# Kernel optimization log

Measured on AMD Instinct MI355X. Metric: run time of the kernel, lower is better.

The kernel has to match this reference:

```python
import jax, jax.numpy as jnp
import numpy as np

B, S = 1, 2560
DIM, NH, HD = 1536, 12, 128
F, HH, WW = 4, 20, 32        # F*HH*WW == S (video latent grid)
EPS = 1e-6
C = HD // 2                  # 64 rotary pairs per head
TD = C - 2 * (C // 3)        # 22 temporal rotary dims
SD = C // 3                  # 21 spatial rotary dims (h and w each)


def setup_inputs() -> dict:
    key = jax.random.key(0)
    ks = jax.random.split(key, 4)
    x = jax.random.normal(ks[0], (B, S, DIM), jnp.float32)
    # Wan-style 3D RoPE angle table: angle[pos, j] = pos * inv_freq_j,
    # segments [0:TD]=temporal, [TD:TD+SD]=height, [TD+SD:]=width.
    def inv(n):
        return 1.0 / (10000.0 ** (np.arange(n, dtype=np.float64) / n))
    inv_full = np.concatenate([inv(TD), inv(SD), inv(SD)])
    freqs = jnp.asarray(np.arange(1024)[:, None] * inv_full[None, :], jnp.float32)
    seq_lens = jnp.full((B,), S, jnp.int32)
    grid_sizes = jnp.asarray([[F, HH, WW]], jnp.int32)
    Wqkv = jax.random.normal(ks[1], (DIM, 3 * DIM), jnp.float32) * 0.02
    bqkv = jnp.zeros((3 * DIM,), jnp.float32)
    gq = jnp.ones((DIM,), jnp.float32)
    gk = jnp.ones((DIM,), jnp.float32)
    Wo = jax.random.normal(ks[2], (DIM, DIM), jnp.float32) * 0.02
    bo = jnp.zeros((DIM,), jnp.float32)
    return dict(x=x, seq_lens=seq_lens, grid_sizes=grid_sizes, freqs=freqs,
                Wqkv=Wqkv, bqkv=bqkv, gq=gq, gk=gk, Wo=Wo, bo=bo)


def _rms(x, g):
    xf = x.astype(jnp.float32)
    y = xf * jax.lax.rsqrt(jnp.mean(xf * xf, axis=-1, keepdims=True) + EPS)
    return (y * g).astype(x.dtype)


def _rope3d(x, freqs):
    # x: [B,S,NH,HD]; rotate adjacent (even,odd) pairs by grid-position angles.
    idx = jnp.arange(S)
    f = idx // (HH * WW)
    h = (idx // WW) % HH
    w = idx % WW
    ang = jnp.concatenate([freqs[f, :TD], freqs[h, TD:TD + SD], freqs[w, TD + SD:]], axis=-1)  # [S, C]
    cos = jnp.cos(ang)[None, :, None, :]
    sin = jnp.sin(ang)[None, :, None, :]
    xr, xi = x[..., 0::2], x[..., 1::2]
    out = jnp.stack([xr * cos - xi * sin, xr * sin + xi * cos], axis=-1)
    return out.reshape(x.shape)


def reference(x, seq_lens, grid_sizes, freqs, Wqkv, bqkv, gq, gk, Wo, bo):
    qkv = x @ Wqkv + bqkv                              # [B,S,3*DIM]
    q, k, v = jnp.split(qkv, 3, axis=-1)
    q = _rms(q, gq).reshape(B, S, NH, HD)
    k = _rms(k, gk).reshape(B, S, NH, HD)
    v = v.reshape(B, S, NH, HD)
    q = _rope3d(q, freqs)
    k = _rope3d(k, freqs)
    scores = jnp.einsum('bsnd,btnd->bnst', q, k) / jnp.sqrt(jnp.float32(HD))
    kmask = (jnp.arange(S)[None, :] < seq_lens[:, None])[:, None, None, :]  # k_lens masking
    scores = jnp.where(kmask, scores, jnp.float32(-1e30))
    attn = jax.nn.softmax(scores, axis=-1)
    out = jnp.einsum('bnst,btnd->bsnd', attn, v).reshape(B, S, DIM)
    return out @ Wo + bo
```

## Files before the change

kernel.cpp:

```cpp
#include <hip/hip_runtime.h>
#include <hip/hip_bf16.h>

constexpr int Sq  = 2560;
constexpr int Dm  = 1536;
constexpr int NHe = 12;
constexpr int HDim= 128;
constexpr int N3c = 4608;
constexpr int TDc = 22;
constexpr int SDc = 21;
constexpr int HHc = 20;
constexpr int WWc = 32;

typedef __attribute__((ext_vector_type(4)))  float f32x4;
typedef __attribute__((ext_vector_type(16))) float f32x16;
typedef __attribute__((ext_vector_type(8)))  short bf16x8;
typedef __attribute__((ext_vector_type(4)))  unsigned u32x4;

__device__ __forceinline__ short f2bf(float f) {
  __hip_bfloat16 h = __float2bfloat16(f);
  return __builtin_bit_cast(short, h);
}
__device__ __forceinline__ float bf2f(short s) {
  __hip_bfloat16 h = __builtin_bit_cast(__hip_bfloat16, s);
  return __bfloat162float(h);
}
__device__ __forceinline__ void gll16(const void* g, void* l) {
  __builtin_amdgcn_global_load_lds((const __attribute__((address_space(1))) unsigned int*)g,
                                   (__attribute__((address_space(3))) unsigned int*)l, 16, 0, 0);
}
__device__ __forceinline__ unsigned cvtpk(float lo, float hi) {
  unsigned r;
  asm("v_cvt_pk_bf16_f32 %0, %1, %2" : "=v"(r) : "v"(lo), "v"(hi));
  return r;
}

__global__ __launch_bounds__(256) void k_convert(const float* __restrict__ in,
                                                 short* __restrict__ out, int n4) {
  int i = blockIdx.x * 256 + threadIdx.x;
  if (i >= n4) return;
  float4 v = reinterpret_cast<const float4*>(in)[i];
  short4 o;
  o.x = f2bf(v.x); o.y = f2bf(v.y); o.z = f2bf(v.z); o.w = f2bf(v.w);
  reinterpret_cast<short4*>(out)[i] = o;
}

__global__ void k_transpose_cvt(const float* __restrict__ in, short* __restrict__ out,
                                int R, int C_) {
  __shared__ float tile[32][33];
  int c0 = blockIdx.x * 32, r0 = blockIdx.y * 32;
  int tx = threadIdx.x, ty = threadIdx.y;
#pragma unroll
  for (int i = 0; i < 4; ++i)
    tile[ty + i * 8][tx] = in[(size_t)(r0 + ty + i * 8) * C_ + c0 + tx];
  __syncthreads();
#pragma unroll
  for (int i = 0; i < 4; ++i)
    out[(size_t)(c0 + ty + i * 8) * R + r0 + tx] = f2bf(tile[tx][ty + i * 8]);
}

__global__ void k_transpose_bf16(const short* __restrict__ in, short* __restrict__ out,
                                 int R, int C_) {
  __shared__ short tile[32][34];
  int h = blockIdx.z;
  const short* ih = in + (size_t)h * R * C_;
  short* oh = out + (size_t)h * R * C_;
  int c0 = blockIdx.x * 32, r0 = blockIdx.y * 32;
  int tx = threadIdx.x, ty = threadIdx.y;
#pragma unroll
  for (int i = 0; i < 4; ++i)
    tile[ty + i * 8][tx] = ih[(size_t)(r0 + ty + i * 8) * C_ + c0 + tx];
  __syncthreads();
#pragma unroll
  for (int i = 0; i < 4; ++i)
    oh[(size_t)(c0 + ty + i * 8) * R + r0 + tx] = tile[tx][ty + i * 8];
}

template <int OUT_BF16, int BM>
__global__ __launch_bounds__(256) void k_gemm_bt(const short* __restrict__ A,
                                                 const short* __restrict__ BT,
                                                 const float* __restrict__ bias,
                                                 void* __restrict__ Cp,
                                                 int M, int N, int K, int ntn) {
  constexpr int MF = BM / 32;
  __shared__ short As[BM * 32];
  __shared__ short Bs[128 * 32];
  int bid = blockIdx.x;
  int mt = bid / ntn, nt = bid % ntn;
  int tid = threadIdx.x, lane = tid & 63, wid = tid >> 6;
  int wr = wid >> 1, wc = wid & 1;
  f32x4 zero = {0.f, 0.f, 0.f, 0.f};
  f32x4 acc[MF][4];
#pragma unroll
  for (int m = 0; m < MF; ++m)
#pragma unroll
    for (int n = 0; n < 4; ++n) acc[m][n] = zero;

  int lrow = lane >> 2;
  int lk8 = (lane & 3) * 8;
  const size_t arow0 = (size_t)mt * BM, brow0 = (size_t)nt * 128;
  int la = lane & 15, lg = lane >> 4;

  for (int kk = 0; kk < K; kk += 32) {
#pragma unroll
    for (int i = 0; i < MF / 2; ++i) {
      int rA = (wid * (MF / 2) + i) * 16 + lrow;
      gll16(A + (arow0 + rA) * K + kk + lk8, As + rA * 32 + lk8);
    }
#pragma unroll
    for (int i = 0; i < 2; ++i) {
      int rB = (wid * 2 + i) * 16 + lrow;
      gll16(BT + (brow0 + rB) * K + kk + lk8, Bs + rB * 32 + lk8);
    }
    __syncthreads();
    bf16x8 af[MF], bfr[4];
#pragma unroll
    for (int m = 0; m < MF; ++m)
      af[m] = *(const bf16x8*)(As + (wr * (BM / 2) + m * 16 + la) * 32 + lg * 8);
#pragma unroll
    for (int n = 0; n < 4; ++n)
      bfr[n] = *(const bf16x8*)(Bs + (wc * 64 + n * 16 + la) * 32 + lg * 8);
#pragma unroll
    for (int m = 0; m < MF; ++m)
#pragma unroll
      for (int n = 0; n < 4; ++n)
        acc[m][n] = __builtin_amdgcn_mfma_f32_16x16x32_bf16(af[m], bfr[n], acc[m][n], 0, 0, 0);
    __syncthreads();
  }
#pragma unroll
  for (int m = 0; m < MF; ++m) {
    int r = (int)arow0 + wr * (BM / 2) + m * 16 + lg * 4;
#pragma unroll
    for (int n = 0; n < 4; ++n) {
      int c = (int)brow0 + wc * 64 + n * 16 + la;
      float b = bias[c];
#pragma unroll
      for (int i = 0; i < 4; ++i) {
        float v = acc[m][n][i] + b;
        if (OUT_BF16) ((short*)Cp)[(size_t)(r + i) * N + c] = f2bf(v);
        else          ((float*)Cp)[(size_t)(r + i) * N + c] = v;
      }
    }
  }
}

__global__ __launch_bounds__(256) void k_rmsrope(const short* __restrict__ qkv,
                                                 const float* __restrict__ freqs,
                                                 const float* __restrict__ gq,
                                                 const float* __restrict__ gk,
                                                 short* __restrict__ Q,
                                                 short* __restrict__ Kx,
                                                 short* __restrict__ V) {
  int s = blockIdx.x;
  const short* row = qkv + (size_t)s * N3c;
  __shared__ float cs[64], sn[64];
  __shared__ float wred[8];
  __shared__ float inv_s[2];
  int tid = threadIdx.x;
  if (tid < 64) {
    int f = s / (HHc * WWc), hh = (s / WWc) % HHc, ww = s % WWc;
    int ridx = tid < TDc ? f : (tid < TDc + SDc ? hh : ww);
    float ang = freqs[ridx * 64 + tid];
    cs[tid] = cosf(ang);
    sn[tid] = sinf(ang);
  }
  float sq = 0.f, sk = 0.f;
  if (tid < 192) {
    bf16x8 a = *(const bf16x8*)(row + tid * 8);
    bf16x8 b = *(const bf16x8*)(row + Dm + tid * 8);
#pragma unroll
    for (int j = 0; j < 8; ++j) {
      float fa = bf2f(a[j]); sq += fa * fa;
      float fb = bf2f(b[j]); sk += fb * fb;
    }
  }
#pragma unroll
  for (int o = 32; o > 0; o >>= 1) { sq += __shfl_down(sq, o); sk += __shfl_down(sk, o); }
  if ((tid & 63) == 0) { wred[tid >> 6] = sq; wred[4 + (tid >> 6)] = sk; }
  __syncthreads();
  if (tid == 0) {
    float a = wred[0] + wred[1] + wred[2] + wred[3];
    float b = wred[4] + wred[5] + wred[6] + wred[7];
    inv_s[0] = rsqrtf(a * (1.0f / Dm) + 1e-6f);
    inv_s[1] = rsqrtf(b * (1.0f / Dm) + 1e-6f);
  }
  __syncthreads();
  float invq = inv_s[0], invk = inv_s[1];
  const float qscale = 0.12751763f;
  for (int p = tid; p < NHe * 64; p += 256) {
    int hd = p >> 6, i = p & 63;
    float c = cs[i], sn_ = sn[i];
    int col = hd * HDim + 2 * i;
    size_t obase = ((size_t)hd * Sq + s) * HDim + 2 * i;
    float xr = bf2f(row[col])     * invq * gq[col];
    float xi = bf2f(row[col + 1]) * invq * gq[col + 1];
    Q[obase]     = f2bf((xr * c - xi * sn_) * qscale);
    Q[obase + 1] = f2bf((xr * sn_ + xi * c) * qscale);
    float yr = bf2f(row[Dm + col])     * invk * gk[col];
    float yi = bf2f(row[Dm + col + 1]) * invk * gk[col + 1];
    Kx[obase]     = f2bf(yr * c - yi * sn_);
    Kx[obase + 1] = f2bf(yr * sn_ + yi * c);
    V[obase]     = row[2 * Dm + col];
    V[obase + 1] = row[2 * Dm + col + 1];
  }
}

__global__ __launch_bounds__(256, 2) void k_attn(const short* __restrict__ Q,
                                                 const short* __restrict__ Kg,
                                                 const short* __restrict__ VT,
                                                 short* __restrict__ O) {
  __shared__ short Xb[2][64 * 128];
  __shared__ short Yb[2][64 * 128];
  __shared__ float Lsh[4][32];
  constexpr int NT = (Sq / 2) / 64;
  int bid = (blockIdx.x & 7) * 60 + (blockIdx.x >> 3);
  int h = bid / 40;
  int q0 = (bid % 40) * 64;
  int tid = threadIdx.x, lane = tid & 63, wid = tid >> 6;
  int qw = wid & 1, kw = wid >> 1;
  int la = lane & 31, hi = lane >> 5;
  const short* Qh = Q  + (size_t)h * Sq * HDim;
  const short* Kh = Kg + (size_t)h * Sq * HDim;
  const short* Vh = VT + (size_t)h * HDim * Sq;
  int qb = q0 + qw * 32;
  int tz = kw * (Sq / 2);
  short* X = Xb[kw];
  short* Y = Yb[kw];

  int koff[8], voff[8], ldo[8];
  const short* Kt = Kh + (size_t)tz * HDim;
  const short* Vt = Vh + tz;
#pragma unroll
  for (int i = 0; i < 8; ++i) {
    int off = (qw * 8 + i) * 1024 + lane * 16;
    int r  = off >> 8, cb  = off & 255;
    koff[i] = r * HDim + ((cb ^ ((r & 15) << 4)) >> 1);
    int r2 = off >> 7, cb2 = off & 127;
    voff[i] = r2 * Sq + ((cb2 ^ ((r2 & 7) << 4)) >> 1);
    ldo[i] = off >> 1;
  }
  auto stageK = [&]() {
#pragma unroll
    for (int i = 0; i < 8; ++i) gll16(Kt + koff[i], X + ldo[i]);
    Kt += 64 * HDim;
  };
  auto stageV = [&]() {
#pragma unroll
    for (int i = 0; i < 8; ++i) gll16(Vt + voff[i], Y + ldo[i]);
    Vt += 64;
  };

  stageK();

  bf16x8 qf[8];
#pragma unroll
  for (int dc = 0; dc < 8; ++dc)
    qf[dc] = *(const bf16x8*)(Qh + (size_t)(qb + la) * HDim + dc * 16 + hi * 8);

  f32x16 o0, o1, o2, o3;
#pragma unroll
  for (int r = 0; r < 16; ++r) { o0[r] = 0.f; o1[r] = 0.f; o2[r] = 0.f; o3[r] = 0.f; }
  float lsum = 0.f;
  const float M2 = 11.5415603f;

  __syncthreads();

  for (int t = 0; t < NT; ++t) {
    stageV();

    f32x16 s0, s1;
#pragma unroll
    for (int r = 0; r < 16; ++r) { s0[r] = 0.f; s1[r] = 0.f; }
    int kcb = ((la & 15) << 4);
#pragma unroll
    for (int dc = 0; dc < 8; ++dc) {
      int bc = (dc * 32 + hi * 16) ^ kcb;
      bf16x8 k0 = *(const bf16x8*)(X + la * 128 + (bc >> 1));
      bf16x8 k1 = *(const bf16x8*)(X + (32 + la) * 128 + (bc >> 1));
      s0 = __builtin_amdgcn_mfma_f32_32x32x16_bf16(k0, qf[dc], s0, 0, 0, 0);
      s1 = __builtin_amdgcn_mfma_f32_32x32x16_bf16(k1, qf[dc], s1, 0, 0, 0);
    }

    float p0[16], p1[16];
#pragma unroll
    for (int r = 0; r < 16; ++r) { p0[r] = exp2f(s0[r] - M2); p1[r] = exp2f(s1[r] - M2); }
    float a0 = 0.f, a1 = 0.f, a2 = 0.f, a3 = 0.f;
#pragma unroll
    for (int m = 0; m < 4; ++m) {
      a0 += p0[m]; a1 += p0[4 + m]; a2 += p0[8 + m]; a3 += p0[12 + m];
      a0 += p1[m]; a1 += p1[4 + m]; a2 += p1[8 + m]; a3 += p1[12 + m];
    }
    lsum += (a0 + a1) + (a2 + a3);

    unsigned w0[8], w1[8];
#pragma unroll
    for (int m = 0; m < 8; ++m) {
      w0[m] = cvtpk(p0[2 * m], p0[2 * m + 1]);
      w1[m] = cvtpk(p1[2 * m], p1[2 * m + 1]);
    }
    unsigned paw[4][4];
#pragma unroll
    for (int tcl = 0; tcl < 2; ++tcl)
#pragma unroll
      for (int jl = 0; jl < 2; ++jl) {
        unsigned A0 = w0[4 * tcl + jl], B0 = w0[4 * tcl + 2 + jl];
        asm("v_permlane32_swap_b32 %0, %1" : "+v"(A0), "+v"(B0));
        paw[tcl][jl] = A0; paw[tcl][2 + jl] = B0;
        unsigned A1 = w1[4 * tcl + jl], B1 = w1[4 * tcl + 2 + jl];
        asm("v_permlane32_swap_b32 %0, %1" : "+v"(A1), "+v"(B1));
        paw[2 + tcl][jl] = A1; paw[2 + tcl][2 + jl] = B1;
      }
    bf16x8 pa[4];
#pragma unroll
    for (int tc = 0; tc < 4; ++tc) {
      u32x4 tw = {paw[tc][0], paw[tc][1], paw[tc][2], paw[tc][3]};
      pa[tc] = __builtin_bit_cast(bf16x8, tw);
    }

    __syncthreads();

    if (t + 1 < NT) stageK();

    int vcb = ((la & 7) << 4);
#pragma unroll
    for (int tc = 0; tc < 4; ++tc) {
      int bc = (tc * 32 + hi * 16) ^ vcb;
      bf16x8 vf0 = *(const bf16x8*)(Y + (la)      * 64 + (bc >> 1));
      bf16x8 vf1 = *(const bf16x8*)(Y + (32 + la) * 64 + (bc >> 1));
      bf16x8 vf2 = *(const bf16x8*)(Y + (64 + la) * 64 + (bc >> 1));
      bf16x8 vf3 = *(const bf16x8*)(Y + (96 + la) * 64 + (bc >> 1));
      o0 = __builtin_amdgcn_mfma_f32_32x32x16_bf16(pa[tc], vf0, o0, 0, 0, 0);
      o1 = __builtin_amdgcn_mfma_f32_32x32x16_bf16(pa[tc], vf1, o1, 0, 0, 0);
      o2 = __builtin_amdgcn_mfma_f32_32x32x16_bf16(pa[tc], vf2, o2, 0, 0, 0);
      o3 = __builtin_amdgcn_mfma_f32_32x32x16_bf16(pa[tc], vf3, o3, 0, 0, 0);
    }
    __syncthreads();
  }

  {
    float A = lsum, B = lsum;
    asm("v_permlane32_swap_b32 %0, %1" : "+v"(A), "+v"(B));
    lsum = A + B;
  }
  if (hi == 0) Lsh[wid][la] = lsum;
  float* fb = (float*)(&Xb[0][0]);
  if (kw == 1) {
    float* dst = fb + qw * 4096 + lane;
#pragma unroll
    for (int r = 0; r < 16; ++r) {
      dst[(r)      * 64] = o0[r];
      dst[(16 + r) * 64] = o1[r];
      dst[(32 + r) * 64] = o2[r];
      dst[(48 + r) * 64] = o3[r];
    }
  }
  __syncthreads();
  if (kw == 0) {
    float ltot = lsum + Lsh[wid + 2][la];
    float rinv = 1.0f / ltot;
    if (hi == 0) Lsh[wid][la] = rinv;
    const float* src = fb + qw * 4096 + lane;
#pragma unroll
    for (int r = 0; r < 16; ++r) {
      o0[r] += src[(r)      * 64];
      o1[r] += src[(16 + r) * 64];
      o2[r] += src[(32 + r) * 64];
      o3[r] += src[(48 + r) * 64];
    }
    float rv[16];
#pragma unroll
    for (int r = 0; r < 16; ++r)
      rv[r] = Lsh[wid][(r & 3) + 8 * (r >> 2) + 4 * hi];
#pragma unroll
    for (int r = 0; r < 16; ++r) {
      int qrow = qb + (r & 3) + 8 * (r >> 2) + 4 * hi;
      short* orow = O + (size_t)qrow * Dm + h * HDim + la;
      orow[0]  = f2bf(o0[r] * rv[r]);
      orow[32] = f2bf(o1[r] * rv[r]);
      orow[64] = f2bf(o2[r] * rv[r]);
      orow[96] = f2bf(o3[r] * rv[r]);
    }
  }
}

extern "C" void kernel_launch(void* const* d_in, const int* in_sizes, int n_in,
                              void* d_out, int out_size, void* d_ws, size_t ws_size,
                              hipStream_t stream) {
  const float* x     = (const float*)d_in[0];
  const float* freqs = (const float*)d_in[3];
  const float* Wqkv  = (const float*)d_in[4];
  const float* bqkv  = (const float*)d_in[5];
  const float* gq    = (const float*)d_in[6];
  const float* gk    = (const float*)d_in[7];
  const float* Wo    = (const float*)d_in[8];
  const float* bo    = (const float*)d_in[9];
  float* out = (float*)d_out;

  char* w = (char*)d_ws;
  short* Qb  = (short*)w;
  short* Kb  = Qb + (size_t)Sq * Dm;
  short* Vb  = Kb + (size_t)Sq * Dm;
  short* xb  = Qb;
  short* WqT = Kb;
  size_t off = (size_t)3 * Sq * Dm * 2;
  short* WoT  = (short*)(w + off); off += (size_t)Dm * Dm * 2;
  short* qkvb = (short*)(w + off); off += (size_t)Sq * N3c * 2;
  short* VTb  = (short*)(w + off); off += (size_t)Sq * Dm * 2;
  short* AOb  = (short*)(w + off); off += (size_t)Sq * Dm * 2;

  dim3 tb(32, 8);
  k_convert<<<(Sq * Dm / 4 + 255) / 256, 256, 0, stream>>>(x, xb, Sq * Dm / 4);
  k_transpose_cvt<<<dim3(N3c / 32, Dm / 32), tb, 0, stream>>>(Wqkv, WqT, Dm, N3c);
  k_transpose_cvt<<<dim3(Dm / 32, Dm / 32), tb, 0, stream>>>(Wo, WoT, Dm, Dm);
  k_gemm_bt<1, 128><<<(Sq / 128) * (N3c / 128), 256, 0, stream>>>(xb, WqT, bqkv, qkvb,
                                                                  Sq, N3c, Dm, N3c / 128);
  k_rmsrope<<<Sq, 256, 0, stream>>>(qkvb, freqs, gq, gk, Qb, Kb, Vb);
  k_transpose_bf16<<<dim3(HDim / 32, Sq / 32, NHe), tb, 0, stream>>>(Vb, VTb, Sq, HDim);
  k_attn<<<480, 256, 0, stream>>>(Qb, Kb, VTb, AOb);
  k_gemm_bt<0, 64><<<(Sq / 64) * (Dm / 128), 256, 0, stream>>>(AOb, WoT, bo, out,
                                                               Sq, Dm, Dm, Dm / 128);
}
```

Before: 179.0 us.

## Double-buffer K tiles in LDS and load V fragments directly from global

The attention kernel now double-buffers K tiles in shared memory, prefetching the next tile at the top of each iteration, which removes one barrier per iteration. V is no longer staged through LDS. Each lane loads its V^T fragments straight from global memory into registers, split into two halves around the softmax. s_setprio hints are added around the MFMA blocks. This adds register pressure and uncoalesced-ish global V reads, and both query waves now read the same V from global instead of sharing it through LDS.

Result: slower. 218.8 us (+22.3%).

```diff
diff --git a/kernel.cpp b/kernel.cpp
--- a/kernel.cpp
+++ b/kernel.cpp
@@ -208,8 +208,7 @@
                                                  const short* __restrict__ Kg,
                                                  const short* __restrict__ VT,
                                                  short* __restrict__ O) {
-  __shared__ short Xb[2][64 * 128];
-  __shared__ short Yb[2][64 * 128];
+  __shared__ short Xb[2][2][64 * 128];
   __shared__ float Lsh[4][32];
   constexpr int NT = (Sq / 2) / 64;
   int bid = (blockIdx.x & 7) * 60 + (blockIdx.x >> 3);
@@ -223,38 +222,32 @@
   const short* Vh = VT + (size_t)h * HDim * Sq;
   int qb = q0 + qw * 32;
   int tz = kw * (Sq / 2);
-  short* X = Xb[kw];
-  short* Y = Yb[kw];
-
-  int koff[8], voff[8], ldo[8];
+  short* X0 = Xb[kw][0];
+  short* X1 = Xb[kw][1];
+
+  int koff[8], ldo[8];
   const short* Kt = Kh + (size_t)tz * HDim;
-  const short* Vt = Vh + tz;
 #pragma unroll
   for (int i = 0; i < 8; ++i) {
     int off = (qw * 8 + i) * 1024 + lane * 16;
     int r  = off >> 8, cb  = off & 255;
     koff[i] = r * HDim + ((cb ^ ((r & 15) << 4)) >> 1);
-    int r2 = off >> 7, cb2 = off & 127;
-    voff[i] = r2 * Sq + ((cb2 ^ ((r2 & 7) << 4)) >> 1);
     ldo[i] = off >> 1;
   }
-  auto stageK = [&]() {
-#pragma unroll
-    for (int i = 0; i < 8; ++i) gll16(Kt + koff[i], X + ldo[i]);
-    Kt += 64 * HDim;
+  auto stageK = [&](int t, short* dst) {
+    const short* src = Kt + (size_t)t * (64 * HDim);
+#pragma unroll
+    for (int i = 0; i < 8; ++i) gll16(src + koff[i], dst + ldo[i]);
   };
-  auto stageV = [&]() {
-#pragma unroll
-    for (int i = 0; i < 8; ++i) gll16(Vt + voff[i], Y + ldo[i]);
-    Vt += 64;
-  };
-
-  stageK();
+
+  stageK(0, X0);
 
   bf16x8 qf[8];
 #pragma unroll
   for (int dc = 0; dc < 8; ++dc)
     qf[dc] = *(const bf16x8*)(Qh + (size_t)(qb + la) * HDim + dc * 16 + hi * 8);
+
+  const short* Vbase = Vh + (size_t)la * Sq + tz + hi * 8;
 
   f32x16 o0, o1, o2, o3;
 #pragma unroll
@@ -265,20 +258,32 @@
   __syncthreads();
 
   for (int t = 0; t < NT; ++t) {
-    stageV();
+    const short* Xc = (t & 1) ? X1 : X0;
+    short* Xn = (t & 1) ? X0 : X1;
+    int tn = (t + 1 < NT) ? t + 1 : t;
+    stageK(tn, Xn);
 
     f32x16 s0, s1;
 #pragma unroll
     for (int r = 0; r < 16; ++r) { s0[r] = 0.f; s1[r] = 0.f; }
     int kcb = ((la & 15) << 4);
+    __builtin_amdgcn_s_setprio(1);
 #pragma unroll
     for (int dc = 0; dc < 8; ++dc) {
       int bc = (dc * 32 + hi * 16) ^ kcb;
-      bf16x8 k0 = *(const bf16x8*)(X + la * 128 + (bc >> 1));
-      bf16x8 k1 = *(const bf16x8*)(X + (32 + la) * 128 + (bc >> 1));
+      bf16x8 k0 = *(const bf16x8*)(Xc + la * 128 + (bc >> 1));
+      bf16x8 k1 = *(const bf16x8*)(Xc + (32 + la) * 128 + (bc >> 1));
       s0 = __builtin_amdgcn_mfma_f32_32x32x16_bf16(k0, qf[dc], s0, 0, 0, 0);
       s1 = __builtin_amdgcn_mfma_f32_32x32x16_bf16(k1, qf[dc], s1, 0, 0, 0);
     }
+    __builtin_amdgcn_s_setprio(0);
+
+    bf16x8 vf[4][4];
+#pragma unroll
+    for (int tc = 0; tc < 2; ++tc)
+#pragma unroll
+      for (int db = 0; db < 4; ++db)
+        vf[tc][db] = *(const bf16x8*)(Vbase + (size_t)db * 32 * Sq + t * 64 + tc * 16);
 
     float p0[16], p1[16];
 #pragma unroll
@@ -316,23 +321,22 @@
       pa[tc] = __builtin_bit_cast(bf16x8, tw);
     }
 
-    __syncthreads();
-
-    if (t + 1 < NT) stageK();
-
-    int vcb = ((la & 7) << 4);
+#pragma unroll
+    for (int tc = 2; tc < 4; ++tc)
+#pragma unroll
+      for (int db = 0; db < 4; ++db)
+        vf[tc][db] = *(const bf16x8*)(Vbase + (size_t)db * 32 * Sq + t * 64 + tc * 16);
+
+    __builtin_amdgcn_s_setprio(1);
 #pragma unroll
     for (int tc = 0; tc < 4; ++tc) {
-      int bc = (tc * 32 + hi * 16) ^ vcb;
-      bf16x8 vf0 = *(const bf16x8*)(Y + (la)      * 64 + (bc >> 1));
-      bf16x8 vf1 = *(const bf16x8*)(Y + (32 + la) * 64 + (bc >> 1));
-      bf16x8 vf2 = *(const bf16x8*)(Y + (64 + la) * 64 + (bc >> 1));
-      bf16x8 vf3 = *(const bf16x8*)(Y + (96 + la) * 64 + (bc >> 1));
-      o0 = __builtin_amdgcn_mfma_f32_32x32x16_bf16(pa[tc], vf0, o0, 0, 0, 0);
-      o1 = __builtin_amdgcn_mfma_f32_32x32x16_bf16(pa[tc], vf1, o1, 0, 0, 0);
-      o2 = __builtin_amdgcn_mfma_f32_32x32x16_bf16(pa[tc], vf2, o2, 0, 0, 0);
-      o3 = __builtin_amdgcn_mfma_f32_32x32x16_bf16(pa[tc], vf3, o3, 0, 0, 0);
-    }
+      o0 = __builtin_amdgcn_mfma_f32_32x32x16_bf16(pa[tc], vf[tc][0], o0, 0, 0, 0);
+      o1 = __builtin_amdgcn_mfma_f32_32x32x16_bf16(pa[tc], vf[tc][1], o1, 0, 0, 0);
+      o2 = __builtin_amdgcn_mfma_f32_32x32x16_bf16(pa[tc], vf[tc][2], o2, 0, 0, 0);
+      o3 = __builtin_amdgcn_mfma_f32_32x32x16_bf16(pa[tc], vf[tc][3], o3, 0, 0, 0);
+    }
+    __builtin_amdgcn_s_setprio(0);
+
     __syncthreads();
   }
 
@@ -342,7 +346,7 @@
     lsum = A + B;
   }
   if (hi == 0) Lsh[wid][la] = lsum;
-  float* fb = (float*)(&Xb[0][0]);
+  float* fb = (float*)(&Xb[0][0][0]);
   if (kw == 1) {
     float* dst = fb + qw * 4096 + lane;
 #pragma unroll
```
